# Kernel tuning notes

Measured on AMD Instinct MI355X. Metric: run time of the kernel, lower is better.

## Reference

```python
import jax, jax.numpy as jnp
import numpy as np

B, F = 65536, 300
SIGMA = 2.0
ALPHA = 1.0


def _gaussian_kernel(sigma):
    l = int(np.round(3 * sigma + 1.0))  # 7 for sigma=2
    x = np.linspace(-(l - 1.0) / 2.0, (l - 1.0) / 2.0, l)
    k = np.exp(-0.5 * np.square(x) / np.square(sigma))
    return (k / k.sum()).astype(np.float32)


def setup_inputs() -> dict:
    key = jax.random.key(0)
    fr_funcs = jax.random.normal(key, (B, F), dtype=jnp.float32)
    freqs = np.arange(1, F + 1, dtype=np.float32)
    freqs = (freqs - freqs.min()) / (freqs.max() - freqs.min())
    freqs = freqs * 2.0 - 1.0  # normalized to [-1, 1], as in __init__
    return {
        "fr_funcs": fr_funcs,
        "freqs": jnp.asarray(freqs),
        "kernel": jnp.asarray(_gaussian_kernel(SIGMA)),
    }


def _first_peak_loss(f, freqs):
    # Replicates softlocalmax's first segment.
    # find_peaks on symmetric-padded signal => boundary is a peak iff it
    # strictly exceeds its single neighbor; interior peaks are strict local maxima.
    n = f.shape[0]
    interior = (f[1:-1] > f[:-2]) & (f[1:-1] > f[2:])
    is_peak = jnp.concatenate([f[0:1] > f[1:2], interior, f[-1:] > f[-2:-1]])
    idx = jnp.where(is_peak, jnp.arange(n, dtype=jnp.int32), n)
    two = jnp.sort(idx)[:2]  # first two peak positions (n if absent)
    npeaks = jnp.sum(is_peak.astype(jnp.int32))
    # first segment end: midpoint of first two peaks (int truncation), else n-1
    end = jnp.where(npeaks >= 2, (two[0] + two[1]) // 2, n - 1)
    mask = jnp.arange(n) < end
    logits = jnp.where(mask, f * ALPHA, -jnp.inf)
    w = jax.nn.softmax(logits)  # zeros outside segment == softmax over slice
    softargmax = w @ freqs
    return -softargmax


def reference(fr_funcs, freqs, kernel):
    # Gaussian1DBlur: conv1d with padding='same' (zero padding, odd kernel)
    blurred = jax.lax.conv_general_dilated(
        fr_funcs[:, None, :], kernel[None, None, :], (1,), "SAME"
    )[:, 0]  # (B, F)
    return jax.vmap(_first_peak_loss, in_axes=(0, None))(blurred, freqs)
```

## Files before the change

kernel.cpp:

```cpp
#include <hip/hip_runtime.h>
#include <math.h>

#define NF 300
#define NC 75

__global__ __launch_bounds__(256) void peak_mover_loss_kernel(
    const float* __restrict__ in,
    const float* __restrict__ freqs,
    const float* __restrict__ kw,
    float* __restrict__ out)
{
    const int row = blockIdx.x * blockDim.x + threadIdx.x;
    const float4* rp4 = reinterpret_cast<const float4*>(in + (size_t)row * NF);

    float kk[7];
#pragma unroll
    for (int t = 0; t < 7; ++t) kk[t] = kw[t];

    float c0 = 0.f, c1 = 0.f, c2 = 0.f;
    float4 A = rp4[0], B = rp4[1], C = rp4[2], D = rp4[3];
    float prev1 = -INFINITY, prev2 = -INFINITY;
    int cnt = 0, p0 = 0, p1 = 0;
    int m = 0;
    for (;;) {
        float b0, b1, b2, b3;
        b0 = kk[0]*c0;  b0=fmaf(kk[1],c1 ,b0); b0=fmaf(kk[2],c2 ,b0); b0=fmaf(kk[3],A.x,b0); b0=fmaf(kk[4],A.y,b0); b0=fmaf(kk[5],A.z,b0); b0=fmaf(kk[6],A.w,b0);
        b1 = kk[0]*c1;  b1=fmaf(kk[1],c2 ,b1); b1=fmaf(kk[2],A.x,b1); b1=fmaf(kk[3],A.y,b1); b1=fmaf(kk[4],A.z,b1); b1=fmaf(kk[5],A.w,b1); b1=fmaf(kk[6],B.x,b1);
        b2 = kk[0]*c2;  b2=fmaf(kk[1],A.x,b2); b2=fmaf(kk[2],A.y,b2); b2=fmaf(kk[3],A.z,b2); b2=fmaf(kk[4],A.w,b2); b2=fmaf(kk[5],B.x,b2); b2=fmaf(kk[6],B.y,b2);
        b3 = kk[0]*A.x; b3=fmaf(kk[1],A.y,b3); b3=fmaf(kk[2],A.z,b3); b3=fmaf(kk[3],A.w,b3); b3=fmaf(kk[4],B.x,b3); b3=fmaf(kk[5],B.y,b3); b3=fmaf(kk[6],B.z,b3);

        const int base = 4 * m;
        if (prev1 > prev2 && prev1 > b0) { if (cnt==0) p0=base-1; else if (cnt==1) p1=base-1; ++cnt; }
        if (b0 > prev1 && b0 > b1)       { if (cnt==0) p0=base;   else if (cnt==1) p1=base;   ++cnt; }
        if (b1 > b0 && b1 > b2)          { if (cnt==0) p0=base+1; else if (cnt==1) p1=base+1; ++cnt; }
        if (b2 > b1 && b2 > b3)          { if (cnt==0) p0=base+2; else if (cnt==1) p1=base+2; ++cnt; }
        if (cnt >= 2) break;
        if (m == NC - 1) {
            if (b3 > b2) { if (cnt==0) p0=NF-1; else if (cnt==1) p1=NF-1; ++cnt; }
            break;
        }
        prev2 = b2; prev1 = b3;
        c0 = A.y; c1 = A.z; c2 = A.w;
        A = B; B = C; C = D;
        const int k = m + 4;
        float4 nd = make_float4(0.f, 0.f, 0.f, 0.f);
        if (k < NC) nd = rp4[k];
        D = nd;
        ++m;
    }

    const int end = (cnt >= 2) ? ((p0 + p1) >> 1) : (NF - 1);

    const float fsc = 2.0f / 299.0f;
    c0 = 0.f; c1 = 0.f; c2 = 0.f;
    A = rp4[0]; B = rp4[1]; C = rp4[2]; D = rp4[3];
    float s = 0.f, tt = 0.f;
    m = 0;
    while (4 * m < end) {
        float b0, b1, b2, b3;
        b0 = kk[0]*c0;  b0=fmaf(kk[1],c1 ,b0); b0=fmaf(kk[2],c2 ,b0); b0=fmaf(kk[3],A.x,b0); b0=fmaf(kk[4],A.y,b0); b0=fmaf(kk[5],A.z,b0); b0=fmaf(kk[6],A.w,b0);
        b1 = kk[0]*c1;  b1=fmaf(kk[1],c2 ,b1); b1=fmaf(kk[2],A.x,b1); b1=fmaf(kk[3],A.y,b1); b1=fmaf(kk[4],A.z,b1); b1=fmaf(kk[5],A.w,b1); b1=fmaf(kk[6],B.x,b1);
        b2 = kk[0]*c2;  b2=fmaf(kk[1],A.x,b2); b2=fmaf(kk[2],A.y,b2); b2=fmaf(kk[3],A.z,b2); b2=fmaf(kk[4],A.w,b2); b2=fmaf(kk[5],B.x,b2); b2=fmaf(kk[6],B.y,b2);
        b3 = kk[0]*A.x; b3=fmaf(kk[1],A.y,b3); b3=fmaf(kk[2],A.z,b3); b3=fmaf(kk[3],A.w,b3); b3=fmaf(kk[4],B.x,b3); b3=fmaf(kk[5],B.y,b3); b3=fmaf(kk[6],B.z,b3);

        const int base = 4 * m;
        if (base     < end) { float e=__expf(b0); s+=e; tt=fmaf(e, fmaf((float)(base  ), fsc, -1.f), tt); }
        if (base + 1 < end) { float e=__expf(b1); s+=e; tt=fmaf(e, fmaf((float)(base+1), fsc, -1.f), tt); }
        if (base + 2 < end) { float e=__expf(b2); s+=e; tt=fmaf(e, fmaf((float)(base+2), fsc, -1.f), tt); }
        if (base + 3 < end) { float e=__expf(b3); s+=e; tt=fmaf(e, fmaf((float)(base+3), fsc, -1.f), tt); }

        c0 = A.y; c1 = A.z; c2 = A.w;
        A = B; B = C; C = D;
        const int k = m + 4;
        float4 nd = make_float4(0.f, 0.f, 0.f, 0.f);
        if (k < NC) nd = rp4[k];
        D = nd;
        ++m;
    }

    out[row] = -(tt / s);
}

extern "C" void kernel_launch(void* const* d_in, const int* in_sizes, int n_in,
                              void* d_out, int out_size, void* d_ws, size_t ws_size,
                              hipStream_t stream) {
    const float* fr    = (const float*)d_in[0];
    const float* freqs = (const float*)d_in[1];
    const float* kw    = (const float*)d_in[2];
    float* outp = (float*)d_out;

    const int nrows = in_sizes[0] / NF;
    const int block = 256;
    const int grid  = nrows / block;
    peak_mover_loss_kernel<<<grid, block, 0, stream>>>(fr, freqs, kw, outp);
}
```

Measured before the change: 109.3 us.

## Stage rows in LDS and split each row across 8 lanes with shuffle reductions

Each block now loads 32 rows into shared memory with coalesced float4 loads. Each row is then processed by 8 cooperating lanes, each handling about 10 float4 chunks. Per-lane peak counts and positions are merged with an associative xor-shuffle reduction, and the softmax sums are reduced the same way. This replaces the uncoalesced one-thread-per-row strided global reads and shortens the serial chain per thread. The cost is that the peak search now always scans the full row instead of exiting early, and the halo chunks are recomputed by each lane.

```diff
diff --git a/kernel.cpp b/kernel.cpp
--- a/kernel.cpp
+++ b/kernel.cpp
@@ -3,6 +3,15 @@
 
 #define NF 300
 #define NC 75
+#define ROWS 32
+#define G 8
+#define CPL 10
+
+#define CONV(b0,b1,b2,b3,c0,c1,c2,A,B) \
+    b0 = kk[0]*c0;  b0=fmaf(kk[1],c1 ,b0); b0=fmaf(kk[2],c2 ,b0); b0=fmaf(kk[3],A.x,b0); b0=fmaf(kk[4],A.y,b0); b0=fmaf(kk[5],A.z,b0); b0=fmaf(kk[6],A.w,b0); \
+    b1 = kk[0]*c1;  b1=fmaf(kk[1],c2 ,b1); b1=fmaf(kk[2],A.x,b1); b1=fmaf(kk[3],A.y,b1); b1=fmaf(kk[4],A.z,b1); b1=fmaf(kk[5],A.w,b1); b1=fmaf(kk[6],B.x,b1); \
+    b2 = kk[0]*c2;  b2=fmaf(kk[1],A.x,b2); b2=fmaf(kk[2],A.y,b2); b2=fmaf(kk[3],A.z,b2); b2=fmaf(kk[4],A.w,b2); b2=fmaf(kk[5],B.x,b2); b2=fmaf(kk[6],B.y,b2); \
+    b3 = kk[0]*A.x; b3=fmaf(kk[1],A.y,b3); b3=fmaf(kk[2],A.z,b3); b3=fmaf(kk[3],A.w,b3); b3=fmaf(kk[4],B.x,b3); b3=fmaf(kk[5],B.y,b3); b3=fmaf(kk[6],B.z,b3);
 
 __global__ __launch_bounds__(256) void peak_mover_loss_kernel(
     const float* __restrict__ in,
@@ -10,75 +19,112 @@
     const float* __restrict__ kw,
     float* __restrict__ out)
 {
-    const int row = blockIdx.x * blockDim.x + threadIdx.x;
-    const float4* rp4 = reinterpret_cast<const float4*>(in + (size_t)row * NF);
+    __shared__ __align__(16) float lds[ROWS * NF];
+
+    const int tid = threadIdx.x;
+    const int rowBase = blockIdx.x * ROWS;
+
+    {
+        const float4* gin = reinterpret_cast<const float4*>(in + (size_t)rowBase * NF);
+        float4* l4 = reinterpret_cast<float4*>(lds);
+#pragma unroll
+        for (int i = 0; i < 10; ++i) {
+            const int idx = tid + 256 * i;
+            if (idx < ROWS * NC) l4[idx] = gin[idx];
+        }
+    }
 
     float kk[7];
 #pragma unroll
     for (int t = 0; t < 7; ++t) kk[t] = kw[t];
 
-    float c0 = 0.f, c1 = 0.f, c2 = 0.f;
-    float4 A = rp4[0], B = rp4[1], C = rp4[2], D = rp4[3];
-    float prev1 = -INFINITY, prev2 = -INFINITY;
+    __syncthreads();
+
+    const int g = tid >> 3;
+    const int l = tid & 7;
+    const float4* rp4 = reinterpret_cast<const float4*>(lds + g * NF);
+
+    const int cs = CPL * l;
+    const int nc = (l == G - 1) ? (NC - cs) : CPL;
+
+    float c0, c1, c2, prev1, prev2;
+    if (l == 0) {
+        c0 = c1 = c2 = 0.f; prev1 = prev2 = -INFINITY;
+    } else {
+        const float4 P = rp4[cs - 2];
+        const float4 Q = rp4[cs - 1];
+        const float4 Rv = rp4[cs];
+        float pb0, pb1, pb2, pb3;
+        float pc0 = P.y, pc1 = P.z, pc2 = P.w;
+        CONV(pb0, pb1, pb2, pb3, pc0, pc1, pc2, Q, Rv);
+        (void)pb0; (void)pb1;
+        prev2 = pb2; prev1 = pb3;
+        c0 = Q.y; c1 = Q.z; c2 = Q.w;
+    }
+
     int cnt = 0, p0 = 0, p1 = 0;
-    int m = 0;
-    for (;;) {
+    float4 A = rp4[cs];
+    for (int t = 0; t < nc; ++t) {
+        const int m = cs + t;
+        float4 B = make_float4(0.f, 0.f, 0.f, 0.f);
+        if (m + 1 < NC) B = rp4[m + 1];
         float b0, b1, b2, b3;
-        b0 = kk[0]*c0;  b0=fmaf(kk[1],c1 ,b0); b0=fmaf(kk[2],c2 ,b0); b0=fmaf(kk[3],A.x,b0); b0=fmaf(kk[4],A.y,b0); b0=fmaf(kk[5],A.z,b0); b0=fmaf(kk[6],A.w,b0);
-        b1 = kk[0]*c1;  b1=fmaf(kk[1],c2 ,b1); b1=fmaf(kk[2],A.x,b1); b1=fmaf(kk[3],A.y,b1); b1=fmaf(kk[4],A.z,b1); b1=fmaf(kk[5],A.w,b1); b1=fmaf(kk[6],B.x,b1);
-        b2 = kk[0]*c2;  b2=fmaf(kk[1],A.x,b2); b2=fmaf(kk[2],A.y,b2); b2=fmaf(kk[3],A.z,b2); b2=fmaf(kk[4],A.w,b2); b2=fmaf(kk[5],B.x,b2); b2=fmaf(kk[6],B.y,b2);
-        b3 = kk[0]*A.x; b3=fmaf(kk[1],A.y,b3); b3=fmaf(kk[2],A.z,b3); b3=fmaf(kk[3],A.w,b3); b3=fmaf(kk[4],B.x,b3); b3=fmaf(kk[5],B.y,b3); b3=fmaf(kk[6],B.z,b3);
-
+        CONV(b0, b1, b2, b3, c0, c1, c2, A, B);
         const int base = 4 * m;
         if (prev1 > prev2 && prev1 > b0) { if (cnt==0) p0=base-1; else if (cnt==1) p1=base-1; ++cnt; }
         if (b0 > prev1 && b0 > b1)       { if (cnt==0) p0=base;   else if (cnt==1) p1=base;   ++cnt; }
         if (b1 > b0 && b1 > b2)          { if (cnt==0) p0=base+1; else if (cnt==1) p1=base+1; ++cnt; }
         if (b2 > b1 && b2 > b3)          { if (cnt==0) p0=base+2; else if (cnt==1) p1=base+2; ++cnt; }
-        if (cnt >= 2) break;
-        if (m == NC - 1) {
-            if (b3 > b2) { if (cnt==0) p0=NF-1; else if (cnt==1) p1=NF-1; ++cnt; }
-            break;
-        }
         prev2 = b2; prev1 = b3;
         c0 = A.y; c1 = A.z; c2 = A.w;
-        A = B; B = C; C = D;
-        const int k = m + 4;
-        float4 nd = make_float4(0.f, 0.f, 0.f, 0.f);
-        if (k < NC) nd = rp4[k];
-        D = nd;
-        ++m;
+        A = B;
     }
+    if (l == G - 1 && prev1 > prev2) { if (cnt==0) p0=NF-1; else if (cnt==1) p1=NF-1; ++cnt; }
 
+#pragma unroll
+    for (int o = 1; o < G; o <<= 1) {
+        const int oc = __shfl_xor(cnt, o, G);
+        const int q0 = __shfl_xor(p0, o, G);
+        const int q1 = __shfl_xor(p1, o, G);
+        const bool right = (l & o) != 0;
+        const int Lc = right ? oc : cnt, Rc = right ? cnt : oc;
+        const int L0 = right ? q0 : p0,  R0 = right ? p0 : q0;
+        const int L1 = right ? q1 : p1,  R1 = right ? p1 : q1;
+        p0 = (Lc >= 1) ? L0 : R0;
+        p1 = (Lc >= 2) ? L1 : ((Lc == 1) ? R0 : R1);
+        cnt = min(Lc + Rc, 2);
+    }
     const int end = (cnt >= 2) ? ((p0 + p1) >> 1) : (NF - 1);
 
     const float fsc = 2.0f / 299.0f;
-    c0 = 0.f; c1 = 0.f; c2 = 0.f;
-    A = rp4[0]; B = rp4[1]; C = rp4[2]; D = rp4[3];
     float s = 0.f, tt = 0.f;
-    m = 0;
-    while (4 * m < end) {
-        float b0, b1, b2, b3;
-        b0 = kk[0]*c0;  b0=fmaf(kk[1],c1 ,b0); b0=fmaf(kk[2],c2 ,b0); b0=fmaf(kk[3],A.x,b0); b0=fmaf(kk[4],A.y,b0); b0=fmaf(kk[5],A.z,b0); b0=fmaf(kk[6],A.w,b0);
-        b1 = kk[0]*c1;  b1=fmaf(kk[1],c2 ,b1); b1=fmaf(kk[2],A.x,b1); b1=fmaf(kk[3],A.y,b1); b1=fmaf(kk[4],A.z,b1); b1=fmaf(kk[5],A.w,b1); b1=fmaf(kk[6],B.x,b1);
-        b2 = kk[0]*c2;  b2=fmaf(kk[1],A.x,b2); b2=fmaf(kk[2],A.y,b2); b2=fmaf(kk[3],A.z,b2); b2=fmaf(kk[4],A.w,b2); b2=fmaf(kk[5],B.x,b2); b2=fmaf(kk[6],B.y,b2);
-        b3 = kk[0]*A.x; b3=fmaf(kk[1],A.y,b3); b3=fmaf(kk[2],A.z,b3); b3=fmaf(kk[3],A.w,b3); b3=fmaf(kk[4],B.x,b3); b3=fmaf(kk[5],B.y,b3); b3=fmaf(kk[6],B.z,b3);
-
-        const int base = 4 * m;
-        if (base     < end) { float e=__expf(b0); s+=e; tt=fmaf(e, fmaf((float)(base  ), fsc, -1.f), tt); }
-        if (base + 1 < end) { float e=__expf(b1); s+=e; tt=fmaf(e, fmaf((float)(base+1), fsc, -1.f), tt); }
-        if (base + 2 < end) { float e=__expf(b2); s+=e; tt=fmaf(e, fmaf((float)(base+2), fsc, -1.f), tt); }
-        if (base + 3 < end) { float e=__expf(b3); s+=e; tt=fmaf(e, fmaf((float)(base+3), fsc, -1.f), tt); }
-
-        c0 = A.y; c1 = A.z; c2 = A.w;
-        A = B; B = C; C = D;
-        const int k = m + 4;
-        float4 nd = make_float4(0.f, 0.f, 0.f, 0.f);
-        if (k < NC) nd = rp4[k];
-        D = nd;
-        ++m;
+    if (4 * cs < end) {
+        float d0, d1, d2;
+        if (l == 0) { d0 = d1 = d2 = 0.f; }
+        else { const float4 Q = rp4[cs - 1]; d0 = Q.y; d1 = Q.z; d2 = Q.w; }
+        float4 A2 = rp4[cs];
+        for (int t = 0; t < nc; ++t) {
+            const int m = cs + t;
+            const int base = 4 * m;
+            if (base >= end) break;
+            float4 B = make_float4(0.f, 0.f, 0.f, 0.f);
+            if (m + 1 < NC) B = rp4[m + 1];
+            float b0, b1, b2, b3;
+            CONV(b0, b1, b2, b3, d0, d1, d2, A2, B);
+            if (base     < end) { float e=__expf(b0); s+=e; tt=fmaf(e, fmaf((float)(base  ), fsc, -1.f), tt); }
+            if (base + 1 < end) { float e=__expf(b1); s+=e; tt=fmaf(e, fmaf((float)(base+1), fsc, -1.f), tt); }
+            if (base + 2 < end) { float e=__expf(b2); s+=e; tt=fmaf(e, fmaf((float)(base+2), fsc, -1.f), tt); }
+            if (base + 3 < end) { float e=__expf(b3); s+=e; tt=fmaf(e, fmaf((float)(base+3), fsc, -1.f), tt); }
+            d0 = A2.y; d1 = A2.z; d2 = A2.w;
+            A2 = B;
+        }
     }
-
-    out[row] = -(tt / s);
+#pragma unroll
+    for (int o = 1; o < G; o <<= 1) {
+        s  += __shfl_xor(s,  o, G);
+        tt += __shfl_xor(tt, o, G);
+    }
+    if (l == 0) out[rowBase + g] = -(tt / s);
 }
 
 extern "C" void kernel_launch(void* const* d_in, const int* in_sizes, int n_in,
@@ -91,6 +137,6 @@
 
     const int nrows = in_sizes[0] / NF;
     const int block = 256;
-    const int grid  = nrows / block;
+    const int grid  = nrows / ROWS;
     peak_mover_loss_kernel<<<grid, block, 0, stream>>>(fr, freqs, kw, outp);
 }
```

After: 123.1 us. 1.13x slower.

## Unroll peak search with batched prefetch and cache blurred prefix in registers

Applied to the files above, without the earlier changes.

The peak search now preloads the first 8 float4 chunks of each row, fully unrolls the first 7 steps and keeps the 28 blurred values in a register array. Any further search loads 16 chunks at once to expose more memory-level parallelism. When the segment end falls within the first 28 elements, the softmax pass reuses the cached blurred values instead of reloading and reconvolving the row. This raises register pressure, which may reduce occupancy, and adds a slow fallback path for late second peaks.

```diff
diff --git a/kernel.cpp b/kernel.cpp
--- a/kernel.cpp
+++ b/kernel.cpp
@@ -3,6 +3,14 @@
 
 #define NF 300
 #define NC 75
+
+#define CONV(b0,b1,b2,b3,c0,c1,c2,A,B) \
+    b0 = kk[0]*c0;  b0=fmaf(kk[1],c1 ,b0); b0=fmaf(kk[2],c2 ,b0); b0=fmaf(kk[3],A.x,b0); b0=fmaf(kk[4],A.y,b0); b0=fmaf(kk[5],A.z,b0); b0=fmaf(kk[6],A.w,b0); \
+    b1 = kk[0]*c1;  b1=fmaf(kk[1],c2 ,b1); b1=fmaf(kk[2],A.x,b1); b1=fmaf(kk[3],A.y,b1); b1=fmaf(kk[4],A.z,b1); b1=fmaf(kk[5],A.w,b1); b1=fmaf(kk[6],B.x,b1); \
+    b2 = kk[0]*c2;  b2=fmaf(kk[1],A.x,b2); b2=fmaf(kk[2],A.y,b2); b2=fmaf(kk[3],A.z,b2); b2=fmaf(kk[4],A.w,b2); b2=fmaf(kk[5],B.x,b2); b2=fmaf(kk[6],B.y,b2); \
+    b3 = kk[0]*A.x; b3=fmaf(kk[1],A.y,b3); b3=fmaf(kk[2],A.z,b3); b3=fmaf(kk[3],A.w,b3); b3=fmaf(kk[4],B.x,b3); b3=fmaf(kk[5],B.y,b3); b3=fmaf(kk[6],B.z,b3);
+
+#define PKCHK(J,V) { if (cnt==0) p0=(J); else if (cnt==1) p1=(J); ++cnt; (void)(V); }
 
 __global__ __launch_bounds__(256) void peak_mover_loss_kernel(
     const float* __restrict__ in,
@@ -17,65 +25,95 @@
 #pragma unroll
     for (int t = 0; t < 7; ++t) kk[t] = kw[t];
 
+    float4 ch[8];
+#pragma unroll
+    for (int t = 0; t < 8; ++t) ch[t] = rp4[t];
+
+    float bl[28];
     float c0 = 0.f, c1 = 0.f, c2 = 0.f;
-    float4 A = rp4[0], B = rp4[1], C = rp4[2], D = rp4[3];
     float prev1 = -INFINITY, prev2 = -INFINITY;
     int cnt = 0, p0 = 0, p1 = 0;
-    int m = 0;
-    for (;;) {
+#pragma unroll
+    for (int m = 0; m < 7; ++m) {
         float b0, b1, b2, b3;
-        b0 = kk[0]*c0;  b0=fmaf(kk[1],c1 ,b0); b0=fmaf(kk[2],c2 ,b0); b0=fmaf(kk[3],A.x,b0); b0=fmaf(kk[4],A.y,b0); b0=fmaf(kk[5],A.z,b0); b0=fmaf(kk[6],A.w,b0);
-        b1 = kk[0]*c1;  b1=fmaf(kk[1],c2 ,b1); b1=fmaf(kk[2],A.x,b1); b1=fmaf(kk[3],A.y,b1); b1=fmaf(kk[4],A.z,b1); b1=fmaf(kk[5],A.w,b1); b1=fmaf(kk[6],B.x,b1);
-        b2 = kk[0]*c2;  b2=fmaf(kk[1],A.x,b2); b2=fmaf(kk[2],A.y,b2); b2=fmaf(kk[3],A.z,b2); b2=fmaf(kk[4],A.w,b2); b2=fmaf(kk[5],B.x,b2); b2=fmaf(kk[6],B.y,b2);
-        b3 = kk[0]*A.x; b3=fmaf(kk[1],A.y,b3); b3=fmaf(kk[2],A.z,b3); b3=fmaf(kk[3],A.w,b3); b3=fmaf(kk[4],B.x,b3); b3=fmaf(kk[5],B.y,b3); b3=fmaf(kk[6],B.z,b3);
+        CONV(b0, b1, b2, b3, c0, c1, c2, ch[m], ch[m + 1]);
+        bl[4*m] = b0; bl[4*m+1] = b1; bl[4*m+2] = b2; bl[4*m+3] = b3;
+        const int base = 4 * m;
+        if (prev1 > prev2 && prev1 > b0) PKCHK(base - 1, 0)
+        if (b0 > prev1 && b0 > b1)       PKCHK(base,     0)
+        if (b1 > b0 && b1 > b2)          PKCHK(base + 1, 0)
+        if (b2 > b1 && b2 > b3)          PKCHK(base + 2, 0)
+        prev2 = b2; prev1 = b3;
+        c0 = ch[m].y; c1 = ch[m].z; c2 = ch[m].w;
+    }
+    float4 A4 = ch[7];
 
-        const int base = 4 * m;
-        if (prev1 > prev2 && prev1 > b0) { if (cnt==0) p0=base-1; else if (cnt==1) p1=base-1; ++cnt; }
-        if (b0 > prev1 && b0 > b1)       { if (cnt==0) p0=base;   else if (cnt==1) p1=base;   ++cnt; }
-        if (b1 > b0 && b1 > b2)          { if (cnt==0) p0=base+1; else if (cnt==1) p1=base+1; ++cnt; }
-        if (b2 > b1 && b2 > b3)          { if (cnt==0) p0=base+2; else if (cnt==1) p1=base+2; ++cnt; }
-        if (cnt >= 2) break;
-        if (m == NC - 1) {
-            if (b3 > b2) { if (cnt==0) p0=NF-1; else if (cnt==1) p1=NF-1; ++cnt; }
-            break;
+    int mc = 7;
+#pragma unroll 1
+    while (cnt < 2 && mc < NC) {
+        float4 cc[17];
+        cc[0] = A4;
+#pragma unroll
+        for (int t = 1; t <= 16; ++t) {
+            const int idx = mc + t;
+            float4 v = make_float4(0.f, 0.f, 0.f, 0.f);
+            if (idx < NC) v = rp4[idx];
+            cc[t] = v;
         }
-        prev2 = b2; prev1 = b3;
-        c0 = A.y; c1 = A.z; c2 = A.w;
-        A = B; B = C; C = D;
-        const int k = m + 4;
-        float4 nd = make_float4(0.f, 0.f, 0.f, 0.f);
-        if (k < NC) nd = rp4[k];
-        D = nd;
-        ++m;
+#pragma unroll
+        for (int t = 0; t < 16; ++t) {
+            const int m = mc + t;
+            if (m < NC && cnt < 2) {
+                float b0, b1, b2, b3;
+                CONV(b0, b1, b2, b3, c0, c1, c2, cc[t], cc[t + 1]);
+                const int base = 4 * m;
+                if (prev1 > prev2 && prev1 > b0) PKCHK(base - 1, 0)
+                if (b0 > prev1 && b0 > b1)       PKCHK(base,     0)
+                if (b1 > b0 && b1 > b2)          PKCHK(base + 1, 0)
+                if (b2 > b1 && b2 > b3)          PKCHK(base + 2, 0)
+                if (m == NC - 1 && cnt < 2 && b3 > b2) PKCHK(NF - 1, 0)
+                prev2 = b2; prev1 = b3;
+                c0 = cc[t].y; c1 = cc[t].z; c2 = cc[t].w;
+            }
+        }
+        A4 = cc[16];
+        mc += 16;
     }
 
     const int end = (cnt >= 2) ? ((p0 + p1) >> 1) : (NF - 1);
 
     const float fsc = 2.0f / 299.0f;
-    c0 = 0.f; c1 = 0.f; c2 = 0.f;
-    A = rp4[0]; B = rp4[1]; C = rp4[2]; D = rp4[3];
     float s = 0.f, tt = 0.f;
-    m = 0;
-    while (4 * m < end) {
-        float b0, b1, b2, b3;
-        b0 = kk[0]*c0;  b0=fmaf(kk[1],c1 ,b0); b0=fmaf(kk[2],c2 ,b0); b0=fmaf(kk[3],A.x,b0); b0=fmaf(kk[4],A.y,b0); b0=fmaf(kk[5],A.z,b0); b0=fmaf(kk[6],A.w,b0);
-        b1 = kk[0]*c1;  b1=fmaf(kk[1],c2 ,b1); b1=fmaf(kk[2],A.x,b1); b1=fmaf(kk[3],A.y,b1); b1=fmaf(kk[4],A.z,b1); b1=fmaf(kk[5],A.w,b1); b1=fmaf(kk[6],B.x,b1);
-        b2 = kk[0]*c2;  b2=fmaf(kk[1],A.x,b2); b2=fmaf(kk[2],A.y,b2); b2=fmaf(kk[3],A.z,b2); b2=fmaf(kk[4],A.w,b2); b2=fmaf(kk[5],B.x,b2); b2=fmaf(kk[6],B.y,b2);
-        b3 = kk[0]*A.x; b3=fmaf(kk[1],A.y,b3); b3=fmaf(kk[2],A.z,b3); b3=fmaf(kk[3],A.w,b3); b3=fmaf(kk[4],B.x,b3); b3=fmaf(kk[5],B.y,b3); b3=fmaf(kk[6],B.z,b3);
-
-        const int base = 4 * m;
-        if (base     < end) { float e=__expf(b0); s+=e; tt=fmaf(e, fmaf((float)(base  ), fsc, -1.f), tt); }
-        if (base + 1 < end) { float e=__expf(b1); s+=e; tt=fmaf(e, fmaf((float)(base+1), fsc, -1.f), tt); }
-        if (base + 2 < end) { float e=__expf(b2); s+=e; tt=fmaf(e, fmaf((float)(base+2), fsc, -1.f), tt); }
-        if (base + 3 < end) { float e=__expf(b3); s+=e; tt=fmaf(e, fmaf((float)(base+3), fsc, -1.f), tt); }
-
-        c0 = A.y; c1 = A.z; c2 = A.w;
-        A = B; B = C; C = D;
-        const int k = m + 4;
-        float4 nd = make_float4(0.f, 0.f, 0.f, 0.f);
-        if (k < NC) nd = rp4[k];
-        D = nd;
-        ++m;
+    if (end <= 28) {
+#pragma unroll
+        for (int j = 0; j < 28; ++j) {
+            if (j < end) {
+                const float e = __expf(bl[j]);
+                s += e;
+                tt = fmaf(e, fmaf((float)j, fsc, -1.f), tt);
+            }
+        }
+    } else {
+        float d0 = 0.f, d1 = 0.f, d2 = 0.f;
+        float4 A = rp4[0], B = rp4[1], C = rp4[2], D = rp4[3];
+        int m = 0;
+#pragma unroll 1
+        while (4 * m < end) {
+            float b0, b1, b2, b3;
+            CONV(b0, b1, b2, b3, d0, d1, d2, A, B);
+            const int base = 4 * m;
+            if (base     < end) { float e=__expf(b0); s+=e; tt=fmaf(e, fmaf((float)(base  ), fsc, -1.f), tt); }
+            if (base + 1 < end) { float e=__expf(b1); s+=e; tt=fmaf(e, fmaf((float)(base+1), fsc, -1.f), tt); }
+            if (base + 2 < end) { float e=__expf(b2); s+=e; tt=fmaf(e, fmaf((float)(base+2), fsc, -1.f), tt); }
+            if (base + 3 < end) { float e=__expf(b3); s+=e; tt=fmaf(e, fmaf((float)(base+3), fsc, -1.f), tt); }
+            d0 = A.y; d1 = A.z; d2 = A.w;
+            A = B; B = C; C = D;
+            const int k = m + 4;
+            float4 nd = make_float4(0.f, 0.f, 0.f, 0.f);
+            if (k < NC) nd = rp4[k];
+            D = nd;
+            ++m;
+        }
     }
 
     out[row] = -(tt / s);
```

New measurement: 107.6 us. About the same (-1.5%).
